# Kernel tuning notes

Measured on AMD Instinct MI355X. Metric: run time of the kernel, lower is better.

Reference implementation:

```python
import jax, jax.numpy as jnp
import numpy as np
from jax import lax

B, T, S, J, D = 8, 512, 32, 64, 400
R, MDU, TAGS = 256, 100, 7


def _lstm(x, Wih, Whh, bih, bhh):
    """PyTorch-convention LSTM over x [N,L,Din]; gate order i,f,g,o.
    Returns (hs, cs) each [N,L,R] in scan order (not re-flipped)."""
    N = x.shape[0]
    Rh = Whh.shape[1]
    h0 = jnp.zeros((N, Rh), x.dtype)
    xW = x @ Wih.T + (bih + bhh)  # precompute input projection [N,L,4R]

    def step(carry, xt):
        h, c = carry
        g = xt + h @ Whh.T
        i, f, gg, o = jnp.split(g, 4, axis=-1)
        c = jax.nn.sigmoid(f) * c + jax.nn.sigmoid(i) * jnp.tanh(gg)
        h = jax.nn.sigmoid(o) * jnp.tanh(c)
        return (h, c), (h, c)

    _, (hs, cs) = lax.scan(step, (h0, h0), xW.transpose(1, 0, 2))
    return hs.transpose(1, 0, 2), cs.transpose(1, 0, 2)


def setup_inputs() -> dict:
    key = jax.random.key(0)
    ks = jax.random.split(key, 40)

    def rn(i, shape, s=0.1):
        return s * jax.random.normal(ks[i], shape, jnp.float32)

    inp = {
        'input_text': rn(0, (B, T, D), 1.0),
        'input_syn': rn(1, (B, S, J, D), 1.0),
        'label': jax.random.randint(ks[2], (B, T), 0, TAGS),
        'len_context': jnp.full((B,), T, jnp.int32),
        'len_synopsis': jnp.full((B, S), J, jnp.int32),
    }
    # 6 LSTM parameter sets: context f1/b1 (in=D), synopsis f/b (in=D), modeling f/b (in=4R)
    idx = 3
    for name, din in [('f1', D), ('b1', D), ('sf', D), ('sb', D), ('mf', 4 * R), ('mb', 4 * R)]:
        inp['Wih_' + name] = rn(idx, (4 * R, din)); idx += 1
        inp['Whh_' + name] = rn(idx, (4 * R, R)); idx += 1
        inp['bih_' + name] = rn(idx, (4 * R,)); idx += 1
        inp['bhh_' + name] = rn(idx, (4 * R,)); idx += 1
    inp['W_cWh'] = rn(idx, (MDU, 2 * R)); idx += 1
    inp['W_cWu'] = rn(idx, (MDU, 2 * R)); idx += 1
    inp['W_v'] = rn(idx, (1, MDU)); idx += 1
    inp['W_sWh'] = rn(idx, (2 * R, 2 * R)); idx += 1
    inp['W_sWu'] = rn(idx, (2 * R, 2 * R)); idx += 1
    inp['W_Ws'] = rn(idx, (MDU, 2 * R)); idx += 1
    inp['W_out'] = rn(idx, (TAGS, 6 * R)); idx += 1
    inp['b_out'] = rn(idx, (TAGS,)); idx += 1
    return inp


def reference(input_text, input_syn, label, len_context, len_synopsis,
              Wih_f1, Whh_f1, bih_f1, bhh_f1,
              Wih_b1, Whh_b1, bih_b1, bhh_b1,
              Wih_sf, Whh_sf, bih_sf, bhh_sf,
              Wih_sb, Whh_sb, bih_sb, bhh_sb,
              Wih_mf, Whh_mf, bih_mf, bhh_mf,
              Wih_mb, Whh_mb, bih_mb, bhh_mb,
              W_cWh, W_cWu, W_v, W_sWh, W_sWu, W_Ws, W_out, b_out):
    B_, T_, D_ = input_text.shape
    S_, J_ = input_syn.shape[1], input_syn.shape[2]

    mask = (jnp.arange(T_)[None, :] < len_context[:, None]).astype(input_text.dtype)

    # --- representation layer: manual bi-LSTMCell; backward hiddens kept in scan order ---
    hs_f, cs_f = _lstm(input_text, Wih_f1, Whh_f1, bih_f1, bhh_f1)
    hs_b, cs_b = _lstm(input_text[:, ::-1], Wih_b1, Whh_b1, bih_b1, bhh_b1)
    H = jnp.concatenate([hs_f, hs_b], -1) * mask[..., None]   # [B,T,2R]
    m = jnp.concatenate([cs_f, cs_b], -1) * mask[..., None]   # [B,T,2R]
    x_init = jnp.zeros((B_, 1, 2 * R), input_text.dtype)
    H_full = jnp.concatenate([x_init, H], 1)                  # H_ : [B,T+1,2R]

    # --- synopsis encoder: bi-LSTM final hidden per synopsis sentence ---
    syn = input_syn.reshape(B_ * S_, J_, D_)
    sh_f, _ = _lstm(syn, Wih_sf, Whh_sf, bih_sf, bhh_sf)
    sh_b, _ = _lstm(syn[:, ::-1], Wih_sb, Whh_sb, bih_sb, bhh_sb)
    U = jnp.concatenate([sh_f[:, -1], sh_b[:, -1]], -1).reshape(B_, S_, 2 * R)

    # --- 'ff' co-attention ---
    cWh = H @ W_cWh.T                                          # [B,T,MDU]
    cWu = U @ W_cWu.T                                          # [B,S,MDU]
    z = jnp.tanh(cWh[:, :, None, :] + cWu[:, None, :, :]) @ W_v[0]  # [B,T,S]
    alpha = jax.nn.softmax(z, axis=-1)
    c = jnp.einsum('bts,bsd->btd', alpha, U)                   # [B,T,2R]

    # --- sentinel (ATT_SYN) ---
    Hprev = H_full[:, :T_]                                     # shifted: x_init, H[0..T-2]
    e = jax.nn.sigmoid(Hprev @ W_sWh.T + Hprev @ W_sWu.T)
    s = e * jnp.tanh(m)                                        # [B,T,2R]
    z_hat = jnp.tanh(s @ W_Ws.T + cWh) @ W_v[0]                # [B,T]
    alpha_hat = jax.nn.softmax(jnp.concatenate([z, z_hat[..., None]], -1), axis=-1)
    beta = alpha_hat[:, :, S_:S_ + 1]                          # [B,T,1]
    c_hat = beta * s + (1.0 - beta) * c
    G = jnp.concatenate([H, c_hat], -1)                        # [B,T,4R]

    # --- modeling bi-LSTM (standard aligned outputs) + output projection ---
    mh_f, _ = _lstm(G, Wih_mf, Whh_mf, bih_mf, bhh_mf)
    mh_b, _ = _lstm(G[:, ::-1], Wih_mb, Whh_mb, bih_mb, bhh_mb)
    M = jnp.concatenate([mh_f, mh_b[:, ::-1]], -1)             # [B,T,2R]

    logit = jnp.concatenate([G, M], -1) @ W_out.T + b_out      # [B,T,TAGS]
    return logit
```

## Files before the change

### kernel.cpp

```cpp
#include <hip/hip_runtime.h>
#include <math.h>
#include <stddef.h>


#define BB 8
#define TT 512
#define SS 32
#define JJ 64
#define DD 400
#define RR 256
#define G4 1024
#define H2 512
#define MDU_ 100
#define TAGS_ 7
#define BT (BB*TT)
#define NSEQ (BB*SS)
#define SCH 64
#define MB1 (1024*1024)

typedef __attribute__((ext_vector_type(8))) short short8;
typedef __attribute__((ext_vector_type(4))) float floatx4;
typedef __attribute__((ext_vector_type(4))) unsigned int u32x4;
typedef unsigned short u16;
typedef unsigned int u32;

__device__ __forceinline__ float us2f(u16 u) {
    unsigned int v = ((unsigned int)u) << 16;
    return __builtin_bit_cast(float, v);
}
__device__ __forceinline__ u16 f2us(float f) {
    unsigned int v = __builtin_bit_cast(unsigned int, f);
    v += 0x7FFFu + ((v >> 16) & 1u);
    return (u16)(v >> 16);
}
__device__ __forceinline__ float ldin(const void* p, long i, int bf) {
    return bf ? us2f(((const u16*)p)[i]) : ((const float*)p)[i];
}
__device__ __forceinline__ float sigm(float x) { return 1.0f / (1.0f + expf(-x)); }
__device__ __forceinline__ float sigm_f(float x) { return 1.0f / (1.0f + __expf(-x)); }
__device__ __forceinline__ float tanh_f(float x) {
    float e = __expf(-2.0f * fabsf(x));
    float t = (1.0f - e) / (1.0f + e);
    return copysignf(t, x);
}

__global__ void detect_k(const void* x, int* flag) {
    __shared__ int cnt;
    if (threadIdx.x == 0) cnt = 0;
    __syncthreads();
    u16 lo = ((const u16*)x)[threadIdx.x * 2];
    int e = (lo >> 7) & 0xFF;
    if (e >= 118 && e <= 131) atomicAdd(&cnt, 1);
    __syncthreads();
    if (threadIdx.x == 0) *flag = (cnt > 128) ? 1 : 0;
}
__global__ void castbf_k(const void* src, long off, u16* dst, long n, const int* flag) {
    long i = (long)blockIdx.x * 256 + threadIdx.x;
    if (i < n) dst[i] = (*flag) ? ((const u16*)src)[off + i] : f2us(((const float*)src)[off + i]);
}
__global__ void castf_k(const void* src, float* dst, long n, const int* flag) {
    long i = (long)blockIdx.x * 256 + threadIdx.x;
    if (i < n) dst[i] = ldin(src, i, *flag);
}
__global__ void zero_k(u32* p, long n) {
    long i = (long)blockIdx.x * 256 + threadIdx.x;
    if (i < n) p[i] = 0u;
}
__global__ void bias_sum_k(const void* bih, const void* bhh, float* out, const int* flag) {
    int i = blockIdx.x * 256 + threadIdx.x;
    if (i < G4) out[i] = ldin(bih, i, *flag) + ldin(bhh, i, *flag);
}
__global__ void wsum_k(const void* a, const void* b, u16* o, const int* flag) {
    int i = blockIdx.x * 256 + threadIdx.x;
    if (i < H2 * H2) o[i] = f2us(ldin(a, i, *flag) + ldin(b, i, *flag));
}
__global__ void whh_frag_k(const void* Whh, u16* WF, const int* flag) {
    int i = blockIdx.x * 256 + threadIdx.x;
    if (i >= 4 * 4 * 4 * 8 * 64 * 8) return;
    int j  = i & 7;
    int ln = (i >> 3) & 63;
    int c  = (i >> 9) & 7;
    int t  = (i >> 12) & 3;
    int w  = (i >> 14) & 3;
    int s  = (i >> 16) & 3;
    int n_g = w * 256 + s * 64 + t * 16 + (ln & 15);
    int k   = c * 32 + (ln >> 4) * 8 + j;
    WF[i] = f2us(ldin(Whh, (long)n_g * 256 + k, *flag));
}

#define BM 128
#define BN 128
#define BK 32
#define LDT 40

__global__ __launch_bounds__(256)
void gemm_bt(const u16* __restrict__ A, int lda,
             const u16* __restrict__ W, int ldw,
             void* __restrict__ C, int ldc,
             const float* __restrict__ bias,
             int M, int N, int K, int outBf16)
{
    __shared__ alignas(16) short As[BM * LDT];
    __shared__ alignas(16) short Bs[BN * LDT];
    const int tid  = threadIdx.x;
    const int m0   = blockIdx.y * BM;
    const int n0   = blockIdx.x * BN;
    const int lane = tid & 63;
    const int wave = tid >> 6;
    const int wm   = wave >> 1, wn = wave & 1;
    const int quad = lane >> 4, mrow = lane & 15;

    floatx4 acc[4][4];
#pragma unroll
    for (int i = 0; i < 4; ++i)
#pragma unroll
        for (int j = 0; j < 4; ++j) { floatx4 z4 = {0.f,0.f,0.f,0.f}; acc[i][j] = z4; }

    for (int k0 = 0; k0 < K; k0 += BK) {
#pragma unroll
        for (int cc = 0; cc < 2; ++cc) {
            int c   = tid + cc * 256;
            int row = c >> 2;
            int kc  = (c & 3) << 3;
            int gk  = k0 + kc;
            {
                int gr = m0 + row;
                short8 v;
                if (gr < M && gk + 8 <= K) {
                    v = *(const short8*)(A + (size_t)gr * lda + gk);
                } else {
#pragma unroll
                    for (int e = 0; e < 8; ++e)
                        v[e] = (gr < M && (gk + e) < K) ? (short)A[(size_t)gr * lda + gk + e] : (short)0;
                }
                *(short8*)&As[row * LDT + kc] = v;
            }
            {
                int gn = n0 + row;
                short8 v;
                if (gn < N && gk + 8 <= K) {
                    v = *(const short8*)(W + (size_t)gn * ldw + gk);
                } else {
#pragma unroll
                    for (int e = 0; e < 8; ++e)
                        v[e] = (gn < N && (gk + e) < K) ? (short)W[(size_t)gn * ldw + gk + e] : (short)0;
                }
                *(short8*)&Bs[row * LDT + kc] = v;
            }
        }
        __syncthreads();

        short8 af[4], bf[4];
#pragma unroll
        for (int i = 0; i < 4; ++i)
            af[i] = *(const short8*)&As[(wm * 64 + i * 16 + mrow) * LDT + quad * 8];
#pragma unroll
        for (int j = 0; j < 4; ++j)
            bf[j] = *(const short8*)&Bs[(wn * 64 + j * 16 + mrow) * LDT + quad * 8];
#pragma unroll
        for (int i = 0; i < 4; ++i)
#pragma unroll
            for (int j = 0; j < 4; ++j)
                acc[i][j] = __builtin_amdgcn_mfma_f32_16x16x32_bf16(af[i], bf[j], acc[i][j], 0, 0, 0);
        __syncthreads();
    }

#pragma unroll
    for (int i = 0; i < 4; ++i)
#pragma unroll
        for (int j = 0; j < 4; ++j)
#pragma unroll
            for (int r = 0; r < 4; ++r) {
                int row = m0 + wm * 64 + i * 16 + quad * 4 + r;
                int col = n0 + wn * 64 + j * 16 + mrow;
                if (row < M && col < N) {
                    float v = acc[i][j][r];
                    if (bias) v += bias[col];
                    if (outBf16) ((u16*)C)[(size_t)row * ldc + col] = f2us(v);
                    else         ((float*)C)[(size_t)row * ldc + col] = v;
                }
            }
}

__global__ __launch_bounds__(256, 1)
void lstm_coop(const u16* __restrict__ xWf, const u16* __restrict__ xWb,
               const u16* __restrict__ WFf, const u16* __restrict__ WFb,
               int L,
               u16* __restrict__ hOut, int hStride,
               u16* __restrict__ cOut, int cStride,
               const int* __restrict__ lenp,
               int writeAtSource, int lastOnly, int seqBase,
               u32* __restrict__ hx32, u32* __restrict__ flags, int grpBase)
{
    const int s   = blockIdx.x;
    const int dir = blockIdx.y;
    const int bat = blockIdx.z;
    const int nb  = gridDim.z;
    const int tid = threadIdx.x;
    const int wv  = tid >> 6;
    const int ln  = tid & 63;
    const int q   = ln >> 4, m = ln & 15;
    const u16* xW = dir ? xWb : xWf;
    const u16* WF = dir ? WFb : WFf;
    const int grp = grpBase + dir * nb + bat;
    u32* flg = flags + (size_t)grp * 16;
    u32* hx  = hx32 + (size_t)grp * 2048;

    __shared__ float g_s[4 * 8 * 64];

    short8 bw[4][8];
    {
        const u16* wb = WF + ((size_t)(s * 4 + wv) * 32) * 512 + ln * 8;
#pragma unroll
        for (int t4 = 0; t4 < 4; ++t4)
#pragma unroll
            for (int c = 0; c < 8; ++c)
                bw[t4][c] = *(const short8*)(wb + (size_t)(t4 * 8 + c) * 512);
    }

    const int seqU = tid >> 5;
    const int j0   = (tid & 31) * 2;
    const int gcol = s * 64 + j0;
    const int mylen = lenp ? lenp[bat * 8 + seqU] : 0x7fffffff;
    float cR0 = 0.f, cR1 = 0.f;

    u32 px0, px1, px2, px3;
    {
        const int tt0 = dir ? (L - 1) : 0;
        const u16* xr = xW + (((size_t)(bat * 8 + seqU)) * L + tt0) * G4 + gcol;
        px0 = *(const u32*)xr;
        px1 = *(const u32*)(xr + 256);
        px2 = *(const u32*)(xr + 512);
        px3 = *(const u32*)(xr + 768);
    }

    for (int t = 0; t < L; ++t) {
        const int tt = dir ? (L - 1 - t) : t;
        short8 a[8];
        if (t > 0) {
            const u32* hp = hx + ((t - 1) & 1) * 1024 + m * 128;
#pragma unroll
            for (int c = 0; c < 8; ++c) {
                if (m < 8) {
                    u32x4 v = *(const u32x4*)(hp + c * 16 + q * 4);
                    a[c] = __builtin_bit_cast(short8, v);
                } else {
                    short8 z = {0,0,0,0,0,0,0,0}; a[c] = z;
                }
            }
        } else {
            short8 z = {0,0,0,0,0,0,0,0};
#pragma unroll
            for (int c = 0; c < 8; ++c) a[c] = z;
        }
        floatx4 acc[4];
#pragma unroll
        for (int t4 = 0; t4 < 4; ++t4) { floatx4 z4 = {0.f,0.f,0.f,0.f}; acc[t4] = z4; }
#pragma unroll
        for (int c = 0; c < 8; ++c)
#pragma unroll
            for (int t4 = 0; t4 < 4; ++t4)
                acc[t4] = __builtin_amdgcn_mfma_f32_16x16x32_bf16(a[c], bw[t4][c], acc[t4], 0, 0, 0);
        if (q < 2) {
#pragma unroll
            for (int t4 = 0; t4 < 4; ++t4)
#pragma unroll
                for (int r = 0; r < 4; ++r)
                    g_s[(wv * 8 + q * 4 + r) * 64 + t4 * 16 + m] = acc[t4][r];
        }
        __syncthreads();
        float hn0, hn1, cn0, cn1;
        {
            float i0 = g_s[(0 * 8 + seqU) * 64 + j0]     + us2f((u16)(px0 & 0xffffu));
            float i1 = g_s[(0 * 8 + seqU) * 64 + j0 + 1] + us2f((u16)(px0 >> 16));
            float f0 = g_s[(1 * 8 + seqU) * 64 + j0]     + us2f((u16)(px1 & 0xffffu));
            float f1 = g_s[(1 * 8 + seqU) * 64 + j0 + 1] + us2f((u16)(px1 >> 16));
            float g0 = g_s[(2 * 8 + seqU) * 64 + j0]     + us2f((u16)(px2 & 0xffffu));
            float g1 = g_s[(2 * 8 + seqU) * 64 + j0 + 1] + us2f((u16)(px2 >> 16));
            float o0 = g_s[(3 * 8 + seqU) * 64 + j0]     + us2f((u16)(px3 & 0xffffu));
            float o1 = g_s[(3 * 8 + seqU) * 64 + j0 + 1] + us2f((u16)(px3 >> 16));
            cn0 = sigm_f(f0) * cR0 + sigm_f(i0) * tanh_f(g0);
            cn1 = sigm_f(f1) * cR1 + sigm_f(i1) * tanh_f(g1);
            hn0 = sigm_f(o0) * tanh_f(cn0);
            hn1 = sigm_f(o1) * tanh_f(cn1);
            cR0 = cn0;
            cR1 = cn1;
            u32 hpack = (u32)f2us(hn0) | ((u32)f2us(hn1) << 16);
            __hip_atomic_store(hx + (t & 1) * 1024 + seqU * 128 + (gcol >> 1),
                               hpack, __ATOMIC_RELAXED, __HIP_MEMORY_SCOPE_AGENT);
        }
        asm volatile("s_waitcnt vmcnt(0)" ::: "memory");
        __syncthreads();
        const bool last = (t == L - 1);
        if (tid == 0 && !last)
            __hip_atomic_store(&flg[s], (u32)(t + 1),
                               __ATOMIC_RELEASE, __HIP_MEMORY_SCOPE_AGENT);
        if (!lastOnly) {
            int wr = writeAtSource ? tt : t;
            float mk = (wr >= mylen) ? 0.f : 1.f;
            size_t ro = ((size_t)(bat * 8 + seqU)) * L + wr;
            u32 hp2 = (u32)f2us(hn0 * mk) | ((u32)f2us(hn1 * mk) << 16);
            *(u32*)(hOut + ro * hStride + dir * RR + gcol) = hp2;
            if (cOut) {
                u32 cp2 = (u32)f2us(cn0 * mk) | ((u32)f2us(cn1 * mk) << 16);
                *(u32*)(cOut + ro * cStride + dir * RR + gcol) = cp2;
            }
        } else if (last) {
            size_t ro = (size_t)(seqBase + bat * 8 + seqU);
            u32 hp2 = (u32)f2us(hn0) | ((u32)f2us(hn1) << 16);
            *(u32*)(hOut + ro * hStride + dir * RR + gcol) = hp2;
        }
        if (!last) {
            {
                const int tn = dir ? (L - 2 - t) : (t + 1);
                const u16* xr = xW + (((size_t)(bat * 8 + seqU)) * L + tn) * G4 + gcol;
                px0 = *(const u32*)xr;
                px1 = *(const u32*)(xr + 256);
                px2 = *(const u32*)(xr + 512);
                px3 = *(const u32*)(xr + 768);
            }
            const u32 tgt = (u32)(t + 1);
            long guard = 0;
            for (;;) {
                u32 f0 = __hip_atomic_load(&flg[0], __ATOMIC_RELAXED, __HIP_MEMORY_SCOPE_AGENT);
                u32 f1 = __hip_atomic_load(&flg[1], __ATOMIC_RELAXED, __HIP_MEMORY_SCOPE_AGENT);
                u32 f2 = __hip_atomic_load(&flg[2], __ATOMIC_RELAXED, __HIP_MEMORY_SCOPE_AGENT);
                u32 f3 = __hip_atomic_load(&flg[3], __ATOMIC_RELAXED, __HIP_MEMORY_SCOPE_AGENT);
                if (f0 >= tgt && f1 >= tgt && f2 >= tgt && f3 >= tgt) break;
                if (++guard > (1L << 18)) break;
                if (guard > 16) __builtin_amdgcn_s_sleep(1);
            }
            __builtin_amdgcn_fence(__ATOMIC_ACQUIRE, "agent");
        }
    }
}

__global__ void hprev_k(const u16* __restrict__ G, u16* __restrict__ Hp) {
    int idx = blockIdx.x * 256 + threadIdx.x;
    if (idx < BT * H2) {
        int r = idx >> 9, d = idx & 511;
        int t = r & (TT - 1);
        Hp[idx] = (t == 0) ? (u16)0 : G[(size_t)(r - 1) * G4 + d];
    }
}
__global__ void s_k(const float* __restrict__ e, const u16* __restrict__ mB,
                    u16* __restrict__ sB) {
    int i = blockIdx.x * 256 + threadIdx.x;
    if (i < BT * H2) sB[i] = f2us(sigm(e[i]) * tanhf(us2f(mB[i])));
}
__global__ void z_k(const float* __restrict__ cWh, const float* __restrict__ cWu,
                    const float* __restrict__ Wv, float* __restrict__ z) {
    int idx = blockIdx.x * 256 + threadIdx.x;
    if (idx >= BT * SS) return;
    int r = idx >> 5, s = idx & 31;
    int b = r >> 9;
    const float* ph = cWh + (size_t)r * MDU_;
    const float* pu = cWu + (size_t)(b * SS + s) * MDU_;
    float acc = 0.f;
    for (int j = 0; j < MDU_; ++j) acc += tanhf(ph[j] + pu[j]) * Wv[j];
    z[idx] = acc;
}
__global__ void zhat_k(const float* __restrict__ sW, const float* __restrict__ cWh,
                       const float* __restrict__ Wv, float* __restrict__ zhat) {
    int r = blockIdx.x * 256 + threadIdx.x;
    if (r >= BT) return;
    float acc = 0.f;
    const float* ps = sW + (size_t)r * MDU_;
    const float* ph = cWh + (size_t)r * MDU_;
    for (int j = 0; j < MDU_; ++j) acc += tanhf(ps[j] + ph[j]) * Wv[j];
    zhat[r] = acc;
}
__global__ __launch_bounds__(64)
void attn_mix_k(const float* __restrict__ z, const float* __restrict__ zhat,
                const u16* __restrict__ U, const u16* __restrict__ sB,
                u16* __restrict__ G) {
    int r = blockIdx.x;
    int lane = threadIdx.x;
    int b = r >> 9;
    __shared__ float alpha[SS];
    float zv = (lane < SS) ? z[(size_t)r * SS + lane] : -1e30f;
    float mx = zv;
    for (int o = 32; o > 0; o >>= 1) mx = fmaxf(mx, __shfl_xor(mx, o));
    float ez = (lane < SS) ? expf(zv - mx) : 0.f;
    float s1 = ez;
    for (int o = 32; o > 0; o >>= 1) s1 += __shfl_xor(s1, o);
    float zh = zhat[r];
    float mx2 = fmaxf(mx, zh);
    float denom = s1 * expf(mx - mx2) + expf(zh - mx2);
    float beta = expf(zh - mx2) / denom;
    if (lane < SS) alpha[lane] = ez / s1;
    __syncthreads();
    for (int d = lane; d < H2; d += 64) {
        float cv = 0.f;
#pragma unroll 8
        for (int s2 = 0; s2 < SS; ++s2)
            cv += alpha[s2] * us2f(U[(size_t)(b * SS + s2) * H2 + d]);
        float sv = us2f(sB[(size_t)r * H2 + d]);
        G[(size_t)r * G4 + H2 + d] = f2us(beta * sv + (1.f - beta) * cv);
    }
}
__global__ __launch_bounds__(256)
void logit_k(const u16* __restrict__ G, const u16* __restrict__ Mb,
             const u16* __restrict__ Wout, const float* __restrict__ boutF,
             void* __restrict__ out, const int* __restrict__ flag) {
    int r = blockIdx.x * 4 + (threadIdx.x >> 6);
    if (r >= BT) return;
    int lane = threadIdx.x & 63;
    float acc[TAGS_] = {0, 0, 0, 0, 0, 0, 0};
    for (int k = lane; k < 1536; k += 64) {
        float v = (k < G4) ? us2f(G[(size_t)r * G4 + k]) : us2f(Mb[(size_t)r * H2 + (k - G4)]);
#pragma unroll
        for (int tg = 0; tg < TAGS_; ++tg) acc[tg] += v * us2f(Wout[tg * 1536 + k]);
    }
#pragma unroll
    for (int tg = 0; tg < TAGS_; ++tg) {
        float s = acc[tg];
        for (int o = 32; o > 0; o >>= 1) s += __shfl_xor(s, o);
        acc[tg] = s;
    }
    if (lane == 0) {
        int bf = *flag;
#pragma unroll
        for (int tg = 0; tg < TAGS_; ++tg) {
            float v = acc[tg] + boutF[tg];
            if (bf) ((u16*)out)[(size_t)r * TAGS_ + tg] = f2us(v);
            else    ((float*)out)[(size_t)r * TAGS_ + tg] = v;
        }
    }
}

extern "C" void kernel_launch(void* const* d_in, const int* in_sizes, int n_in,
                              void* d_out, int out_size, void* d_ws, size_t ws_size,
                              hipStream_t stream)
{
    const void* x_text = d_in[0];
    const void* x_syn  = d_in[1];
    const int* len_ctx = (const int*)d_in[3];
    const void *Wih[6], *Whh[6], *bih[6], *bhh[6];
    for (int l = 0; l < 6; ++l) {
        Wih[l] = d_in[5 + l * 4 + 0];
        Whh[l] = d_in[5 + l * 4 + 1];
        bih[l] = d_in[5 + l * 4 + 2];
        bhh[l] = d_in[5 + l * 4 + 3];
    }
    const void* W_cWh = d_in[29];
    const void* W_cWu = d_in[30];
    const void* W_v   = d_in[31];
    const void* W_sWh = d_in[32];
    const void* W_sWu = d_in[33];
    const void* W_Ws  = d_in[34];
    const void* W_out = d_in[35];
    const void* b_out = d_in[36];
    (void)in_sizes; (void)n_in; (void)out_size;

    char* ws = (char*)d_ws;
    size_t off = 0;
    auto alloc = [&](size_t bytes) -> void* {
        void* p = ws + off;
        off += (bytes + 255) & ~(size_t)255;
        return p;
    };
    int*   flagB  = (int*)alloc(256);
    float* bsum[6];
    for (int l = 0; l < 6; ++l) bsum[l] = (float*)alloc((size_t)G4 * 4);
    u16*   WsumB  = (u16*)alloc((size_t)H2 * H2 * 2);
    u16*   Ub     = (u16*)alloc((size_t)NSEQ * H2 * 2);
    u16*   Gb     = (u16*)alloc((size_t)BT * G4 * 2);
    u16*   mMb    = (u16*)alloc((size_t)BT * H2 * 2);
    float* cWhB   = (float*)alloc((size_t)BT * MDU_ * 4);
    float* cWuB   = (float*)alloc((size_t)NSEQ * MDU_ * 4);
    float* sWB    = (float*)alloc((size_t)BT * MDU_ * 4);
    float* zB     = (float*)alloc((size_t)BT * SS * 4);
    float* zhatB  = (float*)alloc((size_t)BT * 4);
    u16*   Wcwh16 = (u16*)alloc((size_t)MDU_ * H2 * 2);
    u16*   Wcwu16 = (u16*)alloc((size_t)MDU_ * H2 * 2);
    u16*   Wws16  = (u16*)alloc((size_t)MDU_ * H2 * 2);
    u16*   Wout16 = (u16*)alloc((size_t)TAGS_ * 1536 * 2);
    float* WvF    = (float*)alloc((size_t)MDU_ * 4);
    float* boutF  = (float*)alloc((size_t)TAGS_ * 4);
    u16*   WF[6];
    for (int l = 0; l < 6; ++l) WF[l] = (u16*)alloc((size_t)G4 * RR * 2);
    u32*   cnts   = (u32*)alloc((size_t)128 * 16 * 4);
    u32*   hx32   = (u32*)alloc((size_t)128 * 2048 * 4);

    size_t fixedEnd = off;
    bool bigws = (ws_size >= fixedEnd + (size_t)81 * MB1);
    char* BIG = (char*)alloc(bigws ? (size_t)80 * MB1 : (size_t)24 * MB1);

    u16*   bufA  = (u16*)BIG;
    u16*   bufB  = (u16*)(BIG + (size_t)8 * MB1);
    u16*   x16   = (u16*)(BIG + (size_t)16 * MB1);
    u16*   W16a  = (u16*)(BIG + (size_t)19 * MB1 + MB1 / 2);
    u16*   W16b  = (u16*)(BIG + (size_t)20 * MB1 + MB1 / 2);
    u16*   HprevB = (u16*)BIG;
    float* eBuf   = (float*)(BIG + (size_t)4 * MB1);
    u16*   sBuf   = (u16*)(BIG + (size_t)12 * MB1);
    u16*   mxWf  = (u16*)BIG;
    u16*   mxWb  = (u16*)(BIG + (size_t)8 * MB1);
    u16*   W16aD = (u16*)(BIG + (size_t)16 * MB1);
    u16*   W16bD = (u16*)(BIG + (size_t)18 * MB1);
    u16*   mbufA = (u16*)BIG;
    u16*   mbufB = (u16*)(BIG + (size_t)32 * MB1);
    u16*   mx16  = (u16*)(BIG + (size_t)64 * MB1);
    u16*   mW16a = (u16*)(BIG + (size_t)78 * MB1);
    u16*   mW16b = (u16*)(BIG + (size_t)79 * MB1);

    auto cgrid = [](long n) { return dim3((unsigned)((n + 255) / 256)); };

    detect_k<<<dim3(1), dim3(256), 0, stream>>>(x_text, flagB);
    zero_k<<<cgrid(128 * 16), dim3(256), 0, stream>>>(cnts, 128 * 16);
    castbf_k<<<cgrid(MDU_ * H2), dim3(256), 0, stream>>>(W_cWh, 0, Wcwh16, MDU_ * H2, flagB);
    castbf_k<<<cgrid(MDU_ * H2), dim3(256), 0, stream>>>(W_cWu, 0, Wcwu16, MDU_ * H2, flagB);
    castbf_k<<<cgrid(MDU_ * H2), dim3(256), 0, stream>>>(W_Ws, 0, Wws16, MDU_ * H2, flagB);
    castbf_k<<<cgrid(TAGS_ * 1536), dim3(256), 0, stream>>>(W_out, 0, Wout16, TAGS_ * 1536, flagB);
    castf_k<<<cgrid(MDU_), dim3(256), 0, stream>>>(W_v, WvF, MDU_, flagB);
    castf_k<<<cgrid(TAGS_), dim3(256), 0, stream>>>(b_out, boutF, TAGS_, flagB);
    for (int l = 0; l < 6; ++l) {
        bias_sum_k<<<dim3(4), dim3(256), 0, stream>>>(bih[l], bhh[l], bsum[l], flagB);
        whh_frag_k<<<dim3(1024), dim3(256), 0, stream>>>(Whh[l], WF[l], flagB);
    }
    wsum_k<<<cgrid(H2 * H2), dim3(256), 0, stream>>>(W_sWh, W_sWu, WsumB, flagB);

    if (bigws) {
        castbf_k<<<cgrid(G4 * DD), dim3(256), 0, stream>>>(Wih[2], 0, mW16a, G4 * DD, flagB);
        castbf_k<<<cgrid(G4 * DD), dim3(256), 0, stream>>>(Wih[3], 0, mW16b, G4 * DD, flagB);
        castbf_k<<<cgrid((long)NSEQ * JJ * DD), dim3(256), 0, stream>>>(x_syn, 0, mx16, (long)NSEQ * JJ * DD, flagB);
        gemm_bt<<<dim3(8, (NSEQ * JJ) / BM), dim3(256), 0, stream>>>(mx16, DD, mW16a, DD, mbufA, G4, bsum[2], NSEQ * JJ, G4, DD, 1);
        gemm_bt<<<dim3(8, (NSEQ * JJ) / BM), dim3(256), 0, stream>>>(mx16, DD, mW16b, DD, mbufB, G4, bsum[3], NSEQ * JJ, G4, DD, 1);
        lstm_coop<<<dim3(4, 2, 32), dim3(256), 0, stream>>>(
            mbufA, mbufB, WF[2], WF[3], JJ,
            Ub, H2, (u16*)nullptr, 0, (const int*)nullptr,
            0, 1, 0, hx32, cnts, 4);
    } else {
        castbf_k<<<cgrid(G4 * DD), dim3(256), 0, stream>>>(Wih[2], 0, W16a, G4 * DD, flagB);
        castbf_k<<<cgrid(G4 * DD), dim3(256), 0, stream>>>(Wih[3], 0, W16b, G4 * DD, flagB);
        for (int c = 0; c < NSEQ / SCH; ++c) {
            long chunkElems = (long)SCH * JJ * DD;
            castbf_k<<<cgrid(chunkElems), dim3(256), 0, stream>>>(x_syn, (long)c * chunkElems, x16, chunkElems, flagB);
            gemm_bt<<<dim3(8, (SCH * JJ) / BM), dim3(256), 0, stream>>>(x16, DD, W16a, DD, bufA, G4, bsum[2], SCH * JJ, G4, DD, 1);
            gemm_bt<<<dim3(8, (SCH * JJ) / BM), dim3(256), 0, stream>>>(x16, DD, W16b, DD, bufB, G4, bsum[3], SCH * JJ, G4, DD, 1);
            lstm_coop<<<dim3(4, 2, 8), dim3(256), 0, stream>>>(
                bufA, bufB, WF[2], WF[3], JJ,
                Ub, H2, (u16*)nullptr, 0, (const int*)nullptr,
                0, 1, c * SCH, hx32, cnts, 4 + c * 16);
        }
    }

    castbf_k<<<cgrid((long)BT * DD), dim3(256), 0, stream>>>(x_text, 0, x16, (long)BT * DD, flagB);
    castbf_k<<<cgrid(G4 * DD), dim3(256), 0, stream>>>(Wih[0], 0, W16a, G4 * DD, flagB);
    castbf_k<<<cgrid(G4 * DD), dim3(256), 0, stream>>>(Wih[1], 0, W16b, G4 * DD, flagB);
    gemm_bt<<<dim3(8, 32), dim3(256), 0, stream>>>(x16, DD, W16a, DD, bufA, G4, bsum[0], BT, G4, DD, 1);
    gemm_bt<<<dim3(8, 32), dim3(256), 0, stream>>>(x16, DD, W16b, DD, bufB, G4, bsum[1], BT, G4, DD, 1);
    lstm_coop<<<dim3(4, 2, 1), dim3(256), 0, stream>>>(
        bufA, bufB, WF[0], WF[1], TT,
        Gb, G4, mMb, H2, len_ctx, 0, 0, 0, hx32, cnts, 0);

    gemm_bt<<<dim3(1, 32), dim3(256), 0, stream>>>(Gb, G4, Wcwh16, H2, cWhB, MDU_, nullptr, BT, MDU_, H2, 0);
    gemm_bt<<<dim3(1, 2),  dim3(256), 0, stream>>>(Ub, H2, Wcwu16, H2, cWuB, MDU_, nullptr, NSEQ, MDU_, H2, 0);
    hprev_k<<<cgrid(BT * H2), dim3(256), 0, stream>>>(Gb, HprevB);
    gemm_bt<<<dim3(4, 32), dim3(256), 0, stream>>>(HprevB, H2, WsumB, H2, eBuf, H2, nullptr, BT, H2, H2, 0);
    s_k<<<cgrid(BT * H2), dim3(256), 0, stream>>>(eBuf, mMb, sBuf);
    gemm_bt<<<dim3(1, 32), dim3(256), 0, stream>>>(sBuf, H2, Wws16, H2, sWB, MDU_, nullptr, BT, MDU_, H2, 0);
    z_k<<<cgrid(BT * SS), dim3(256), 0, stream>>>(cWhB, cWuB, WvF, zB);
    zhat_k<<<cgrid(BT), dim3(256), 0, stream>>>(sWB, cWhB, WvF, zhatB);
    attn_mix_k<<<dim3(BT), dim3(64), 0, stream>>>(zB, zhatB, Ub, sBuf, Gb);

    castbf_k<<<cgrid(G4 * G4), dim3(256), 0, stream>>>(Wih[4], 0, W16aD, G4 * G4, flagB);
    castbf_k<<<cgrid(G4 * G4), dim3(256), 0, stream>>>(Wih[5], 0, W16bD, G4 * G4, flagB);
    gemm_bt<<<dim3(8, 32), dim3(256), 0, stream>>>(Gb, G4, W16aD, G4, mxWf, G4, bsum[4], BT, G4, G4, 1);
    gemm_bt<<<dim3(8, 32), dim3(256), 0, stream>>>(Gb, G4, W16bD, G4, mxWb, G4, bsum[5], BT, G4, G4, 1);
    lstm_coop<<<dim3(4, 2, 1), dim3(256), 0, stream>>>(
        mxWf, mxWb, WF[4], WF[5], TT,
        mMb, H2, (u16*)nullptr, 0, (const int*)nullptr, 1, 0, 0, hx32, cnts, 2);

    logit_k<<<dim3(BT / 4), dim3(256), 0, stream>>>(Gb, mMb, Wout16, boutF, d_out, flagB);
}
```

Before: 4.932 ms.

## Co-locate LSTM slice blocks on one XCD and pad and single-thread the step flags

The recurrent LSTM kernel now uses a flat 1-D grid. Blocks are laid out so that the four hidden-slice workgroups of each (direction, batch) group sit G8 apart. With round-robin dispatch across XCDs, that should place them on the same XCD and let them exchange per-step h values and flags through a shared L2. Each slice's step flag is padded to its own 64-byte line, and only thread 0 spins on the flags before a block barrier, which cuts polling traffic. In exchange, the kernel launches idle padding blocks that exit at once, and it relies on dispatch-order assumptions that the hardware does not guarantee.

```diff
diff --git a/kernel.cpp b/kernel.cpp
--- a/kernel.cpp
+++ b/kernel.cpp
@@ -190,20 +190,23 @@
                u16* __restrict__ cOut, int cStride,
                const int* __restrict__ lenp,
                int writeAtSource, int lastOnly, int seqBase,
-               u32* __restrict__ hx32, u32* __restrict__ flags, int grpBase)
+               u32* __restrict__ hx32, u32* __restrict__ flags,
+               int grpBase, int nb, int G8)
 {
-    const int s   = blockIdx.x;
-    const int dir = blockIdx.y;
-    const int bat = blockIdx.z;
-    const int nb  = gridDim.z;
+    const int wgid = blockIdx.x;
+    const int s    = wgid / G8;
+    const int g    = wgid - s * G8;
+    if (g >= 2 * nb) return;
+    const int dir  = g / nb;
+    const int bat  = g - dir * nb;
     const int tid = threadIdx.x;
     const int wv  = tid >> 6;
     const int ln  = tid & 63;
     const int q   = ln >> 4, m = ln & 15;
     const u16* xW = dir ? xWb : xWf;
     const u16* WF = dir ? WFb : WFf;
-    const int grp = grpBase + dir * nb + bat;
-    u32* flg = flags + (size_t)grp * 16;
+    const int grp = grpBase + g;
+    u32* flg = flags + (size_t)grp * 64;
     u32* hx  = hx32 + (size_t)grp * 2048;
 
     __shared__ float g_s[4 * 8 * 64];
@@ -293,7 +296,7 @@
         __syncthreads();
         const bool last = (t == L - 1);
         if (tid == 0 && !last)
-            __hip_atomic_store(&flg[s], (u32)(t + 1),
+            __hip_atomic_store(&flg[s * 16], (u32)(t + 1),
                                __ATOMIC_RELEASE, __HIP_MEMORY_SCOPE_AGENT);
         if (!lastOnly) {
             int wr = writeAtSource ? tt : t;
@@ -319,18 +322,21 @@
                 px2 = *(const u32*)(xr + 512);
                 px3 = *(const u32*)(xr + 768);
             }
-            const u32 tgt = (u32)(t + 1);
-            long guard = 0;
-            for (;;) {
-                u32 f0 = __hip_atomic_load(&flg[0], __ATOMIC_RELAXED, __HIP_MEMORY_SCOPE_AGENT);
-                u32 f1 = __hip_atomic_load(&flg[1], __ATOMIC_RELAXED, __HIP_MEMORY_SCOPE_AGENT);
-                u32 f2 = __hip_atomic_load(&flg[2], __ATOMIC_RELAXED, __HIP_MEMORY_SCOPE_AGENT);
-                u32 f3 = __hip_atomic_load(&flg[3], __ATOMIC_RELAXED, __HIP_MEMORY_SCOPE_AGENT);
-                if (f0 >= tgt && f1 >= tgt && f2 >= tgt && f3 >= tgt) break;
-                if (++guard > (1L << 18)) break;
-                if (guard > 16) __builtin_amdgcn_s_sleep(1);
-            }
-            __builtin_amdgcn_fence(__ATOMIC_ACQUIRE, "agent");
+            if (tid == 0) {
+                const u32 tgt = (u32)(t + 1);
+                long guard = 0;
+                for (;;) {
+                    u32 f0 = __hip_atomic_load(&flg[0],  __ATOMIC_RELAXED, __HIP_MEMORY_SCOPE_AGENT);
+                    u32 f1 = __hip_atomic_load(&flg[16], __ATOMIC_RELAXED, __HIP_MEMORY_SCOPE_AGENT);
+                    u32 f2 = __hip_atomic_load(&flg[32], __ATOMIC_RELAXED, __HIP_MEMORY_SCOPE_AGENT);
+                    u32 f3 = __hip_atomic_load(&flg[48], __ATOMIC_RELAXED, __HIP_MEMORY_SCOPE_AGENT);
+                    if (f0 >= tgt && f1 >= tgt && f2 >= tgt && f3 >= tgt) break;
+                    if (++guard > (1L << 18)) break;
+                    if (guard > 32) __builtin_amdgcn_s_sleep(1);
+                }
+                __builtin_amdgcn_fence(__ATOMIC_ACQUIRE, "agent");
+            }
+            __syncthreads();
         }
     }
 }
@@ -480,7 +486,7 @@
     float* boutF  = (float*)alloc((size_t)TAGS_ * 4);
     u16*   WF[6];
     for (int l = 0; l < 6; ++l) WF[l] = (u16*)alloc((size_t)G4 * RR * 2);
-    u32*   cnts   = (u32*)alloc((size_t)128 * 16 * 4);
+    u32*   cnts   = (u32*)alloc((size_t)128 * 64 * 4);
     u32*   hx32   = (u32*)alloc((size_t)128 * 2048 * 4);
 
     size_t fixedEnd = off;
@@ -508,7 +514,7 @@
     auto cgrid = [](long n) { return dim3((unsigned)((n + 255) / 256)); };
 
     detect_k<<<dim3(1), dim3(256), 0, stream>>>(x_text, flagB);
-    zero_k<<<cgrid(128 * 16), dim3(256), 0, stream>>>(cnts, 128 * 16);
+    zero_k<<<cgrid(128 * 64), dim3(256), 0, stream>>>(cnts, 128 * 64);
     castbf_k<<<cgrid(MDU_ * H2), dim3(256), 0, stream>>>(W_cWh, 0, Wcwh16, MDU_ * H2, flagB);
     castbf_k<<<cgrid(MDU_ * H2), dim3(256), 0, stream>>>(W_cWu, 0, Wcwu16, MDU_ * H2, flagB);
     castbf_k<<<cgrid(MDU_ * H2), dim3(256), 0, stream>>>(W_Ws, 0, Wws16, MDU_ * H2, flagB);
@@ -527,10 +533,10 @@
         castbf_k<<<cgrid((long)NSEQ * JJ * DD), dim3(256), 0, stream>>>(x_syn, 0, mx16, (long)NSEQ * JJ * DD, flagB);
         gemm_bt<<<dim3(8, (NSEQ * JJ) / BM), dim3(256), 0, stream>>>(mx16, DD, mW16a, DD, mbufA, G4, bsum[2], NSEQ * JJ, G4, DD, 1);
         gemm_bt<<<dim3(8, (NSEQ * JJ) / BM), dim3(256), 0, stream>>>(mx16, DD, mW16b, DD, mbufB, G4, bsum[3], NSEQ * JJ, G4, DD, 1);
-        lstm_coop<<<dim3(4, 2, 32), dim3(256), 0, stream>>>(
+        lstm_coop<<<dim3(256), dim3(256), 0, stream>>>(
             mbufA, mbufB, WF[2], WF[3], JJ,
             Ub, H2, (u16*)nullptr, 0, (const int*)nullptr,
-            0, 1, 0, hx32, cnts, 4);
+            0, 1, 0, hx32, cnts, 4, 32, 64);
     } else {
         castbf_k<<<cgrid(G4 * DD), dim3(256), 0, stream>>>(Wih[2], 0, W16a, G4 * DD, flagB);
         castbf_k<<<cgrid(G4 * DD), dim3(256), 0, stream>>>(Wih[3], 0, W16b, G4 * DD, flagB);
@@ -539,10 +545,10 @@
             castbf_k<<<cgrid(chunkElems), dim3(256), 0, stream>>>(x_syn, (long)c * chunkElems, x16, chunkElems, flagB);
             gemm_bt<<<dim3(8, (SCH * JJ) / BM), dim3(256), 0, stream>>>(x16, DD, W16a, DD, bufA, G4, bsum[2], SCH * JJ, G4, DD, 1);
             gemm_bt<<<dim3(8, (SCH * JJ) / BM), dim3(256), 0, stream>>>(x16, DD, W16b, DD, bufB, G4, bsum[3], SCH * JJ, G4, DD, 1);
-            lstm_coop<<<dim3(4, 2, 8), dim3(256), 0, stream>>>(
+            lstm_coop<<<dim3(64), dim3(256), 0, stream>>>(
                 bufA, bufB, WF[2], WF[3], JJ,
                 Ub, H2, (u16*)nullptr, 0, (const int*)nullptr,
-                0, 1, c * SCH, hx32, cnts, 4 + c * 16);
+                0, 1, c * SCH, hx32, cnts, 4 + c * 16, 8, 16);
         }
     }
 
@@ -551,9 +557,9 @@
     castbf_k<<<cgrid(G4 * DD), dim3(256), 0, stream>>>(Wih[1], 0, W16b, G4 * DD, flagB);
     gemm_bt<<<dim3(8, 32), dim3(256), 0, stream>>>(x16, DD, W16a, DD, bufA, G4, bsum[0], BT, G4, DD, 1);
     gemm_bt<<<dim3(8, 32), dim3(256), 0, stream>>>(x16, DD, W16b, DD, bufB, G4, bsum[1], BT, G4, DD, 1);
-    lstm_coop<<<dim3(4, 2, 1), dim3(256), 0, stream>>>(
+    lstm_coop<<<dim3(32), dim3(256), 0, stream>>>(
         bufA, bufB, WF[0], WF[1], TT,
-        Gb, G4, mMb, H2, len_ctx, 0, 0, 0, hx32, cnts, 0);
+        Gb, G4, mMb, H2, len_ctx, 0, 0, 0, hx32, cnts, 0, 1, 8);
 
     gemm_bt<<<dim3(1, 32), dim3(256), 0, stream>>>(Gb, G4, Wcwh16, H2, cWhB, MDU_, nullptr, BT, MDU_, H2, 0);
     gemm_bt<<<dim3(1, 2),  dim3(256), 0, stream>>>(Ub, H2, Wcwu16, H2, cWuB, MDU_, nullptr, NSEQ, MDU_, H2, 0);
@@ -569,9 +575,9 @@
     castbf_k<<<cgrid(G4 * G4), dim3(256), 0, stream>>>(Wih[5], 0, W16bD, G4 * G4, flagB);
     gemm_bt<<<dim3(8, 32), dim3(256), 0, stream>>>(Gb, G4, W16aD, G4, mxWf, G4, bsum[4], BT, G4, G4, 1);
     gemm_bt<<<dim3(8, 32), dim3(256), 0, stream>>>(Gb, G4, W16bD, G4, mxWb, G4, bsum[5], BT, G4, G4, 1);
-    lstm_coop<<<dim3(4, 2, 1), dim3(256), 0, stream>>>(
+    lstm_coop<<<dim3(32), dim3(256), 0, stream>>>(
         mxWf, mxWb, WF[4], WF[5], TT,
-        mMb, H2, (u16*)nullptr, 0, (const int*)nullptr, 1, 0, 0, hx32, cnts, 2);
+        mMb, H2, (u16*)nullptr, 0, (const int*)nullptr, 1, 0, 0, hx32, cnts, 2, 1, 8);
 
     logit_k<<<dim3(BT / 4), dim3(256), 0, stream>>>(Gb, mMb, Wout16, boutF, d_out, flagB);
 }
```

Result: faster. 4.183 ms (-15.2%).
